# Kernel optimization log

Measured on AMD Instinct MI355X. Metric: run time of the kernel, lower is better.

## Reference

```python
import jax, jax.numpy as jnp
import numpy as np

B, P = 32, 1024
HID, H, D = 512, 8, 64   # hidden_dim, heads, head_dim
MEM, RANK = 64, 64


def setup_inputs() -> dict:
    key = jax.random.key(0)
    ks = jax.random.split(key, 12)
    s1 = 1.0  # Linear(1, hidden): fan_in = 1 -> torch init bound = 1
    sh = 1.0 / np.sqrt(HID)
    sd = 1.0 / np.sqrt(D)
    return {
        "x":    jax.random.normal(ks[0], (B, P), dtype=jnp.float32),
        # q/k/v: Linear(1, hidden) -> weight (hidden,), bias (hidden,)
        "w_q": jax.random.uniform(ks[1], (HID,), jnp.float32, -s1, s1),
        "b_q": jax.random.uniform(ks[2], (HID,), jnp.float32, -s1, s1),
        "w_k": jax.random.uniform(ks[3], (HID,), jnp.float32, -s1, s1),
        "b_k": jax.random.uniform(ks[4], (HID,), jnp.float32, -s1, s1),
        "w_v": jax.random.uniform(ks[5], (HID,), jnp.float32, -s1, s1),
        "b_v": jax.random.uniform(ks[6], (HID,), jnp.float32, -s1, s1),
        # mem_proj: Linear(head_dim, mem_size, bias=False) -> weight (mem, d)
        "w_mem": jax.random.uniform(ks[7], (MEM, D), jnp.float32, -sd, sd),
        # project_to_U / V: Linear(hidden, rank)
        "w_u":  jax.random.uniform(ks[8], (RANK, HID), jnp.float32, -sh, sh),
        "b_u":  jax.random.uniform(ks[9], (RANK,), jnp.float32, -sh, sh),
        "w_v2": jax.random.uniform(ks[10], (RANK, HID), jnp.float32, -sh, sh),
        "b_v2": jax.random.uniform(ks[11], (RANK,), jnp.float32, -sh, sh),
    }


def reference(x, w_q, b_q, w_k, b_k, w_v, b_v, w_mem, w_u, b_u, w_v2, b_v2):
    Bx, p = x.shape
    xu = x[..., None]                                  # (B, p, 1)
    # Linear(1, hidden) is a scalar broadcast: x * w + b
    def to_heads(w, b):
        y = xu * w + b                                 # (B, p, HID)
        return y.reshape(Bx, p, H, D).transpose(0, 2, 1, 3)  # (B, H, p, D)
    Q = to_heads(w_q, b_q)
    K = to_heads(w_k, b_k)
    V = to_heads(w_v, b_v)

    phi = lambda u: jax.nn.elu(u) + 1.0
    Qf = phi(Q)                                        # (B, H, p, D)
    # memory weights: softmax over the p axis (dim=2)
    W_mem = jax.nn.softmax(jnp.einsum('bhpd,md->bhpm', K, w_mem), axis=2)
    mem_KV = jnp.einsum('bhpm,bhpd->bhmd', W_mem, V)   # (B, H, MEM, D)
    attn = jnp.einsum('bhpd,bhmd->bhpm', Qf, mem_KV)   # (B, H, p, MEM)
    h = jnp.einsum('bhpm,bhmd->bhpd', attn, mem_KV)    # (B, H, p, D)
    h = h.transpose(0, 2, 1, 3).reshape(Bx, p, H * D)  # (B, p, HID)

    U = h @ w_u.T + b_u                                # (B, p, RANK)
    Vp = h @ w_v2.T + b_v2                             # (B, p, RANK)
    coeffs_k = jnp.einsum('bpr,bqr->bpq', U, Vp)       # (B, p, p)
    return coeffs_k
```

## Files before the change

### kernel.cpp

```cpp
#include <hip/hip_runtime.h>
#include <hip/hip_bf16.h>

#define BB 32
#define PP 1024
#define HID 512
#define NH 8
#define DD 64
#define MEM 64
#define RANK 64

#define A_OFF   0
#define M_OFF   512
#define T_OFF   1024
#define S1_OFF  17408
#define S2_OFF  17664
#define G_OFF   18432
#define F_OFF   542720

__global__ __launch_bounds__(1024) void k_precompute(
    const float* __restrict__ wk, const float* __restrict__ wmem,
    const float* __restrict__ wv, const float* __restrict__ bv,
    const float* __restrict__ wu, const float* __restrict__ bu,
    const float* __restrict__ wv2, const float* __restrict__ bv2,
    float* __restrict__ A, float* __restrict__ M17) {
  __shared__ float WU[17 * 64];
  __shared__ float WV[17 * 64];
  const int t = threadIdx.x;

  if (t < 512) {
    const int h = t >> 6, m = t & 63;
    float s = 0.f;
    for (int d = 0; d < DD; ++d) s += wk[h * DD + d] * wmem[m * DD + d];
    A[t] = s;
  }

  for (int i = t; i < 17 * 64; i += 1024) {
    const int j = i >> 6, r = i & 63;
    float su = 0.f, sv = 0.f;
    if (j < 8) {
      for (int d = 0; d < DD; ++d) {
        const float w = wv[j * DD + d];
        su += wu[r * HID + j * DD + d] * w;
        sv += wv2[r * HID + j * DD + d] * w;
      }
    } else if (j < 16) {
      const int h = j - 8;
      for (int d = 0; d < DD; ++d) {
        const float w = bv[h * DD + d];
        su += wu[r * HID + h * DD + d] * w;
        sv += wv2[r * HID + h * DD + d] * w;
      }
    } else {
      su = bu[r];
      sv = bv2[r];
    }
    WU[i] = su;
    WV[i] = sv;
  }
  __syncthreads();

  if (t < 17 * 17) {
    const int i = t / 17, j = t % 17;
    float s = 0.f;
    for (int r = 0; r < 64; ++r) s += WU[i * 64 + r] * WV[j * 64 + r];
    M17[t] = s;
  }
}

__global__ __launch_bounds__(256) void k_memsoftmax(
    const float* __restrict__ x, const float* __restrict__ A,
    float* __restrict__ T) {
  const int wid = blockIdx.x * 4 + (threadIdx.x >> 6);
  const int lane = threadIdx.x & 63;
  const int b = wid >> 9;
  const int hm = wid & 511;
  const float a = A[hm];
  const float* xr = x + b * PP;

  float xs[16];
  float mx = -INFINITY;
#pragma unroll
  for (int k = 0; k < 16; ++k) {
    xs[k] = xr[lane + k * 64];
    mx = fmaxf(mx, xs[k] * a);
  }
#pragma unroll
  for (int off = 32; off >= 1; off >>= 1) mx = fmaxf(mx, __shfl_xor(mx, off));

  float s = 0.f, sx = 0.f;
#pragma unroll
  for (int k = 0; k < 16; ++k) {
    const float e = __expf(xs[k] * a - mx);
    s += e;
    sx += e * xs[k];
  }
#pragma unroll
  for (int off = 32; off >= 1; off >>= 1) {
    s += __shfl_xor(s, off);
    sx += __shfl_xor(sx, off);
  }
  if (lane == 0) T[wid] = sx / s;
}

__global__ __launch_bounds__(256) void k_tsums(
    const float* __restrict__ T, float* __restrict__ S1,
    float* __restrict__ S2) {
  const int t = threadIdx.x;
  const float* Tr = T + t * MEM;
  float s1 = 0.f, s2 = 0.f;
  for (int m = 0; m < MEM; ++m) {
    const float v = Tr[m];
    s1 += v;
    s2 += v * v;
  }
  S1[t] = s1;
  S2[t] = s2;
}

__global__ __launch_bounds__(256) void k_features(
    const float* __restrict__ x, const float* __restrict__ wq,
    const float* __restrict__ bq, const float* __restrict__ wv,
    const float* __restrict__ bv, const float* __restrict__ S1,
    const float* __restrict__ S2, float* __restrict__ G) {
  const int idx0 = blockIdx.x * 256;
  const int b = idx0 >> 13;
  const int h = (idx0 >> 10) & 7;
  const int p = (idx0 & 1023) + threadIdx.x;

  const float xv = x[b * PP + p];
  float a1 = 0.f, a0 = 0.f;
#pragma unroll 8
  for (int d = 0; d < DD; ++d) {
    const float q = xv * wq[h * DD + d] + bq[h * DD + d];
    const float ph = (q > 0.f) ? (q + 1.f) : __expf(q);
    a1 += ph * wv[h * DD + d];
    a0 += ph * bv[h * DD + d];
  }
  const float s1 = S1[b * 8 + h], s2 = S2[b * 8 + h];
  const float c1 = a1 * s2 + a0 * s1;
  const float c2 = a1 * s1 + a0 * (float)MEM;
  G[(b * 16 + h) * PP + p] = c1;
  G[(b * 16 + 8 + h) * PP + p] = c2;
}

__global__ __launch_bounds__(256) void k_fmap(
    const float* __restrict__ G, const float* __restrict__ M17,
    float* __restrict__ F) {
  __shared__ float Ml[17 * 17];
  const int t = threadIdx.x;
  for (int i = t; i < 17 * 17; i += 256) Ml[i] = M17[i];
  __syncthreads();

  const int idx = blockIdx.x * 256 + t;
  const int b = idx >> 10, p = idx & 1023;
  float g[16];
#pragma unroll
  for (int i = 0; i < 16; ++i) g[i] = G[(b * 16 + i) * PP + p];
#pragma unroll
  for (int j = 0; j < 17; ++j) {
    float f = Ml[16 * 17 + j];
#pragma unroll
    for (int i = 0; i < 16; ++i) f += g[i] * Ml[i * 17 + j];
    F[(b * 17 + j) * PP + p] = f;
  }
}

__global__ __launch_bounds__(256) void k_coeffs(
    const float* __restrict__ F, const float* __restrict__ G,
    float* __restrict__ out) {
  __shared__ float Fl[17 * 64];
  __shared__ float Gl[16 * 64];
  const int b = blockIdx.z;
  const int p0 = blockIdx.y * 64;
  const int q0 = blockIdx.x * 64;
  const int t = threadIdx.x;

  const float* Fg = F + (size_t)b * 17 * PP;
  const float* Gg = G + (size_t)b * 16 * PP;
  for (int i = t; i < 17 * 64; i += 256) Fl[i] = Fg[(i >> 6) * PP + p0 + (i & 63)];
  for (int i = t; i < 16 * 64; i += 256) Gl[i] = Gg[(i >> 6) * PP + q0 + (i & 63)];
  __syncthreads();

  const int pr = t >> 4;
  const int qv = t & 15;

  const float4 f16 = *(const float4*)&Fl[16 * 64 + pr * 4];
  float4 acc0 = make_float4(f16.x, f16.x, f16.x, f16.x);
  float4 acc1 = make_float4(f16.y, f16.y, f16.y, f16.y);
  float4 acc2 = make_float4(f16.z, f16.z, f16.z, f16.z);
  float4 acc3 = make_float4(f16.w, f16.w, f16.w, f16.w);

#pragma unroll
  for (int j = 0; j < 16; ++j) {
    const float4 fj = *(const float4*)&Fl[j * 64 + pr * 4];
    const float4 gj = *(const float4*)&Gl[j * 64 + qv * 4];
    acc0.x += fj.x * gj.x; acc0.y += fj.x * gj.y; acc0.z += fj.x * gj.z; acc0.w += fj.x * gj.w;
    acc1.x += fj.y * gj.x; acc1.y += fj.y * gj.y; acc1.z += fj.y * gj.z; acc1.w += fj.y * gj.w;
    acc2.x += fj.z * gj.x; acc2.y += fj.z * gj.y; acc2.z += fj.z * gj.z; acc2.w += fj.z * gj.w;
    acc3.x += fj.w * gj.x; acc3.y += fj.w * gj.y; acc3.z += fj.w * gj.z; acc3.w += fj.w * gj.w;
  }

  const size_t base = ((size_t)(b * PP + p0 + pr * 4)) * PP + q0 + qv * 4;
  *(float4*)&out[base] = acc0;
  *(float4*)&out[base + PP] = acc1;
  *(float4*)&out[base + 2 * PP] = acc2;
  *(float4*)&out[base + 3 * PP] = acc3;
}

extern "C" void kernel_launch(void* const* d_in, const int* in_sizes, int n_in,
                              void* d_out, int out_size, void* d_ws, size_t ws_size,
                              hipStream_t stream) {
  const float* x    = (const float*)d_in[0];
  const float* wq   = (const float*)d_in[1];
  const float* bq   = (const float*)d_in[2];
  const float* wk   = (const float*)d_in[3];
  const float* bk   = (const float*)d_in[4];  (void)bk;
  const float* wv   = (const float*)d_in[5];
  const float* bv   = (const float*)d_in[6];
  const float* wmem = (const float*)d_in[7];
  const float* wu   = (const float*)d_in[8];
  const float* bu   = (const float*)d_in[9];
  const float* wv2  = (const float*)d_in[10];
  const float* bv2  = (const float*)d_in[11];

  float* ws = (float*)d_ws;
  float* A   = ws + A_OFF;
  float* M17 = ws + M_OFF;
  float* T   = ws + T_OFF;
  float* S1  = ws + S1_OFF;
  float* S2  = ws + S2_OFF;
  float* G   = ws + G_OFF;
  float* F   = ws + F_OFF;
  float* out = (float*)d_out;

  k_precompute<<<1, 1024, 0, stream>>>(wk, wmem, wv, bv, wu, bu, wv2, bv2, A, M17);
  k_memsoftmax<<<4096, 256, 0, stream>>>(x, A, T);
  k_tsums<<<1, 256, 0, stream>>>(T, S1, S2);
  k_features<<<1024, 256, 0, stream>>>(x, wq, bq, wv, bv, S1, S2, G);
  k_fmap<<<128, 256, 0, stream>>>(G, M17, F);
  k_coeffs<<<dim3(16, 16, 32), 256, 0, stream>>>(F, G, out);
}
```

Measured before the change: 226.4 us.

## Fuse tsums/features/fmap into one kernel and enlarge coeffs tiles to 128x128

Merges the T-sum reduction, per-head feature computation and the 17x17 feature map into a single kernel. Each block reduces its batch's T rows with wave shuffles and computes all 8 heads per position, which removes two launches and the G round trip through global memory. Separately, the output kernel moves from 64x64 to 128x128 tiles, with each thread computing an 8x8 register block instead of 4x4. The fused kernel runs only 128 blocks with an 8x longer loop per thread, and the larger tiles raise register pressure and cut the grid size.

```diff
diff --git a/kernel.cpp b/kernel.cpp
--- a/kernel.cpp
+++ b/kernel.cpp
@@ -12,8 +12,6 @@
 #define A_OFF   0
 #define M_OFF   512
 #define T_OFF   1024
-#define S1_OFF  17408
-#define S2_OFF  17664
 #define G_OFF   18432
 #define F_OFF   542720
 
@@ -102,60 +100,54 @@
   if (lane == 0) T[wid] = sx / s;
 }
 
-__global__ __launch_bounds__(256) void k_tsums(
-    const float* __restrict__ T, float* __restrict__ S1,
-    float* __restrict__ S2) {
-  const int t = threadIdx.x;
-  const float* Tr = T + t * MEM;
-  float s1 = 0.f, s2 = 0.f;
-  for (int m = 0; m < MEM; ++m) {
-    const float v = Tr[m];
-    s1 += v;
-    s2 += v * v;
-  }
-  S1[t] = s1;
-  S2[t] = s2;
-}
-
-__global__ __launch_bounds__(256) void k_features(
+__global__ __launch_bounds__(256) void k_features_fused(
     const float* __restrict__ x, const float* __restrict__ wq,
     const float* __restrict__ bq, const float* __restrict__ wv,
-    const float* __restrict__ bv, const float* __restrict__ S1,
-    const float* __restrict__ S2, float* __restrict__ G) {
-  const int idx0 = blockIdx.x * 256;
-  const int b = idx0 >> 13;
-  const int h = (idx0 >> 10) & 7;
-  const int p = (idx0 & 1023) + threadIdx.x;
-
-  const float xv = x[b * PP + p];
-  float a1 = 0.f, a0 = 0.f;
-#pragma unroll 8
-  for (int d = 0; d < DD; ++d) {
-    const float q = xv * wq[h * DD + d] + bq[h * DD + d];
-    const float ph = (q > 0.f) ? (q + 1.f) : __expf(q);
-    a1 += ph * wv[h * DD + d];
-    a0 += ph * bv[h * DD + d];
-  }
-  const float s1 = S1[b * 8 + h], s2 = S2[b * 8 + h];
-  const float c1 = a1 * s2 + a0 * s1;
-  const float c2 = a1 * s1 + a0 * (float)MEM;
-  G[(b * 16 + h) * PP + p] = c1;
-  G[(b * 16 + 8 + h) * PP + p] = c2;
-}
-
-__global__ __launch_bounds__(256) void k_fmap(
-    const float* __restrict__ G, const float* __restrict__ M17,
+    const float* __restrict__ bv, const float* __restrict__ T,
+    const float* __restrict__ M17, float* __restrict__ G,
     float* __restrict__ F) {
   __shared__ float Ml[17 * 17];
+  __shared__ float s1s[8], s2s[8];
   const int t = threadIdx.x;
+  const int b = blockIdx.x >> 2;
+  const int p = ((blockIdx.x & 3) << 8) + t;
+
   for (int i = t; i < 17 * 17; i += 256) Ml[i] = M17[i];
+
+  const int w = t >> 6, lane = t & 63;
+#pragma unroll
+  for (int hh = w * 2; hh < w * 2 + 2; ++hh) {
+    const float v = T[(b * 8 + hh) * MEM + lane];
+    float s1 = v, s2 = v * v;
+#pragma unroll
+    for (int off = 32; off >= 1; off >>= 1) {
+      s1 += __shfl_xor(s1, off);
+      s2 += __shfl_xor(s2, off);
+    }
+    if (lane == 0) { s1s[hh] = s1; s2s[hh] = s2; }
+  }
   __syncthreads();
 
-  const int idx = blockIdx.x * 256 + t;
-  const int b = idx >> 10, p = idx & 1023;
+  const float xv = x[b * PP + p];
   float g[16];
 #pragma unroll
-  for (int i = 0; i < 16; ++i) g[i] = G[(b * 16 + i) * PP + p];
+  for (int h = 0; h < 8; ++h) {
+    float a1 = 0.f, a0 = 0.f;
+#pragma unroll 8
+    for (int d = 0; d < DD; ++d) {
+      const float q = xv * wq[h * DD + d] + bq[h * DD + d];
+      const float ph = (q > 0.f) ? (q + 1.f) : __expf(q);
+      a1 += ph * wv[h * DD + d];
+      a0 += ph * bv[h * DD + d];
+    }
+    const float s1 = s1s[h], s2 = s2s[h];
+    g[h] = a1 * s2 + a0 * s1;
+    g[8 + h] = a1 * s1 + a0 * (float)MEM;
+  }
+
+#pragma unroll
+  for (int i = 0; i < 16; ++i) G[(b * 16 + i) * PP + p] = g[i];
+
 #pragma unroll
   for (int j = 0; j < 17; ++j) {
     float f = Ml[16 * 17 + j];
@@ -168,43 +160,49 @@
 __global__ __launch_bounds__(256) void k_coeffs(
     const float* __restrict__ F, const float* __restrict__ G,
     float* __restrict__ out) {
-  __shared__ float Fl[17 * 64];
-  __shared__ float Gl[16 * 64];
+  __shared__ float Fl[17 * 128];
+  __shared__ float Gl[16 * 128];
   const int b = blockIdx.z;
-  const int p0 = blockIdx.y * 64;
-  const int q0 = blockIdx.x * 64;
+  const int p0 = blockIdx.y * 128;
+  const int q0 = blockIdx.x * 128;
   const int t = threadIdx.x;
 
   const float* Fg = F + (size_t)b * 17 * PP;
   const float* Gg = G + (size_t)b * 16 * PP;
-  for (int i = t; i < 17 * 64; i += 256) Fl[i] = Fg[(i >> 6) * PP + p0 + (i & 63)];
-  for (int i = t; i < 16 * 64; i += 256) Gl[i] = Gg[(i >> 6) * PP + q0 + (i & 63)];
+  for (int i = t; i < 17 * 128; i += 256) Fl[i] = Fg[(i >> 7) * PP + p0 + (i & 127)];
+  for (int i = t; i < 16 * 128; i += 256) Gl[i] = Gg[(i >> 7) * PP + q0 + (i & 127)];
   __syncthreads();
 
-  const int pr = t >> 4;
-  const int qv = t & 15;
-
-  const float4 f16 = *(const float4*)&Fl[16 * 64 + pr * 4];
-  float4 acc0 = make_float4(f16.x, f16.x, f16.x, f16.x);
-  float4 acc1 = make_float4(f16.y, f16.y, f16.y, f16.y);
-  float4 acc2 = make_float4(f16.z, f16.z, f16.z, f16.z);
-  float4 acc3 = make_float4(f16.w, f16.w, f16.w, f16.w);
+  const int pr = (t >> 4) * 8;
+  const int qc = (t & 15) * 8;
+
+  float acc[8][8];
+#pragma unroll
+  for (int i = 0; i < 8; ++i) {
+    const float f16v = Fl[16 * 128 + pr + i];
+#pragma unroll
+    for (int k = 0; k < 8; ++k) acc[i][k] = f16v;
+  }
 
 #pragma unroll
   for (int j = 0; j < 16; ++j) {
-    const float4 fj = *(const float4*)&Fl[j * 64 + pr * 4];
-    const float4 gj = *(const float4*)&Gl[j * 64 + qv * 4];
-    acc0.x += fj.x * gj.x; acc0.y += fj.x * gj.y; acc0.z += fj.x * gj.z; acc0.w += fj.x * gj.w;
-    acc1.x += fj.y * gj.x; acc1.y += fj.y * gj.y; acc1.z += fj.y * gj.z; acc1.w += fj.y * gj.w;
-    acc2.x += fj.z * gj.x; acc2.y += fj.z * gj.y; acc2.z += fj.z * gj.z; acc2.w += fj.z * gj.w;
-    acc3.x += fj.w * gj.x; acc3.y += fj.w * gj.y; acc3.z += fj.w * gj.z; acc3.w += fj.w * gj.w;
-  }
-
-  const size_t base = ((size_t)(b * PP + p0 + pr * 4)) * PP + q0 + qv * 4;
-  *(float4*)&out[base] = acc0;
-  *(float4*)&out[base + PP] = acc1;
-  *(float4*)&out[base + 2 * PP] = acc2;
-  *(float4*)&out[base + 3 * PP] = acc3;
+    float fj[8], gj[8];
+    *(float4*)&fj[0] = *(const float4*)&Fl[j * 128 + pr];
+    *(float4*)&fj[4] = *(const float4*)&Fl[j * 128 + pr + 4];
+    *(float4*)&gj[0] = *(const float4*)&Gl[j * 128 + qc];
+    *(float4*)&gj[4] = *(const float4*)&Gl[j * 128 + qc + 4];
+#pragma unroll
+    for (int i = 0; i < 8; ++i)
+#pragma unroll
+      for (int k = 0; k < 8; ++k) acc[i][k] += fj[i] * gj[k];
+  }
+
+#pragma unroll
+  for (int i = 0; i < 8; ++i) {
+    const size_t base = ((size_t)(b * PP + p0 + pr + i)) * PP + q0 + qc;
+    *(float4*)&out[base] = make_float4(acc[i][0], acc[i][1], acc[i][2], acc[i][3]);
+    *(float4*)&out[base + 4] = make_float4(acc[i][4], acc[i][5], acc[i][6], acc[i][7]);
+  }
 }
 
 extern "C" void kernel_launch(void* const* d_in, const int* in_sizes, int n_in,
@@ -227,16 +225,12 @@
   float* A   = ws + A_OFF;
   float* M17 = ws + M_OFF;
   float* T   = ws + T_OFF;
-  float* S1  = ws + S1_OFF;
-  float* S2  = ws + S2_OFF;
   float* G   = ws + G_OFF;
   float* F   = ws + F_OFF;
   float* out = (float*)d_out;
 
   k_precompute<<<1, 1024, 0, stream>>>(wk, wmem, wv, bv, wu, bu, wv2, bv2, A, M17);
   k_memsoftmax<<<4096, 256, 0, stream>>>(x, A, T);
-  k_tsums<<<1, 256, 0, stream>>>(T, S1, S2);
-  k_features<<<1024, 256, 0, stream>>>(x, wq, bq, wv, bv, S1, S2, G);
-  k_fmap<<<128, 256, 0, stream>>>(G, M17, F);
-  k_coeffs<<<dim3(16, 16, 32), 256, 0, stream>>>(F, G, out);
-}
+  k_features_fused<<<128, 256, 0, stream>>>(x, wq, bq, wv, bv, T, M17, G, F);
+  k_coeffs<<<dim3(8, 8, 32), 256, 0, stream>>>(F, G, out);
+}
```

Measured after the change: 249.6 us. 1.1x slower.
